# Performance work log

Hardware: AMD Instinct MI355X
Metric: run time of the kernel (lower is better)

Reference implementation:

```python
import jax, jax.numpy as jnp
import numpy as np

NUM_EMBEDDINGS = 8192
EMBEDDING_DIM = 512
COMMITMENT_COST = 0.25
DECAY = 0.99
EPSILON = 1e-05


def _l2_normalize(x, axis=-1, eps=1e-12):
    # matches torch.nn.functional.normalize (p=2)
    n = jnp.sqrt(jnp.sum(x * x, axis=axis, keepdims=True))
    return x / jnp.maximum(n, eps)


def setup_inputs() -> dict:
    key = jax.random.key(0)
    k1, k2, k3 = jax.random.split(key, 3)
    inputs = jax.random.normal(k1, (8, 4096, EMBEDDING_DIM), dtype=jnp.float32)
    embedding = jax.random.normal(k2, (NUM_EMBEDDINGS, EMBEDDING_DIM), dtype=jnp.float32) * 0.01
    ema_cluster_size = jnp.ones((NUM_EMBEDDINGS,), dtype=jnp.float32)
    ema_w = jax.random.normal(k3, (NUM_EMBEDDINGS, EMBEDDING_DIM), dtype=jnp.float32) * 0.01
    return {"inputs": inputs, "embedding": embedding,
            "ema_cluster_size": ema_cluster_size, "ema_w": ema_w}


def reference(inputs, embedding, ema_cluster_size, ema_w):
    K, D = NUM_EMBEDDINGS, EMBEDDING_DIM
    flat = _l2_normalize(inputs.reshape(-1, D))           # [N, D]
    emb_n = _l2_normalize(embedding)                       # [K, D] (in-place normalize in torch)

    # cosine distance: 1 - flat @ emb^T  -> argmin
    distances = 1.0 - jnp.matmul(flat, emb_n.T)            # [N, K]
    idx = jnp.argmin(distances, axis=1)                    # [N]

    # one-hot @ codebook == gather
    quantized = jnp.take(emb_n, idx, axis=0).reshape(inputs.shape)

    # EMA codebook update (training branch), scatter-encode via segment_sum
    counts = jax.ops.segment_sum(jnp.ones_like(idx, dtype=flat.dtype), idx,
                                 num_segments=K)           # [K]
    new_cs = ema_cluster_size * DECAY + (1.0 - DECAY) * counts
    n = jnp.sum(new_cs)
    new_cs = (new_cs + EPSILON) / (n + K * EPSILON) * n
    dw = jax.ops.segment_sum(flat, idx, num_segments=K)    # [K, D] == one_hot^T @ flat
    new_ema_w = ema_w * DECAY + (1.0 - DECAY) * dw
    new_embedding = new_ema_w / jnp.clip(new_cs, EPSILON, None)[:, None]

    e_latent_loss = jnp.mean((jax.lax.stop_gradient(quantized) - inputs) ** 2)
    loss = COMMITMENT_COST * e_latent_loss

    quantized_st = inputs + jax.lax.stop_gradient(quantized - inputs)
    encoding_indices = idx.reshape(inputs.shape[:-1])
    return (quantized_st, loss, encoding_indices, new_cs, new_ema_w, new_embedding)
```

## Files before the change

kernel.cpp:

```cpp
#include <hip/hip_runtime.h>
#include <math.h>

#define NROWS 32768
#define DIM   512
#define KCODE 8192
#define DECAYF 0.99f
#define OMDF   0.01f
#define EPSF   1e-5f
#define COMMITF 0.25f
#define MARGIN 8e-4f

typedef _Float16 half8 __attribute__((ext_vector_type(8)));
typedef _Float16 half4v __attribute__((ext_vector_type(4)));
typedef _Float16 half2v __attribute__((ext_vector_type(2)));
typedef float floatx16 __attribute__((ext_vector_type(16)));


__device__ __forceinline__ float block_sum_256(float v) {
    __shared__ float sm[4];
    int lane = threadIdx.x & 63, wave = threadIdx.x >> 6;
    #pragma unroll
    for (int off = 32; off; off >>= 1) v += __shfl_down(v, off);
    if (lane == 0) sm[wave] = v;
    __syncthreads();
    if (threadIdx.x == 0) v = sm[0] + sm[1] + sm[2] + sm[3];
    return v;
}

__global__ void k_norm_split(const float* __restrict__ src, float* __restrict__ inv,
                             _Float16* __restrict__ hi, _Float16* __restrict__ lo) {
    const int wave = threadIdx.x >> 6;
    const int lane = threadIdx.x & 63;
    const int row = blockIdx.x * 4 + wave;
    const float* p = src + (size_t)row * DIM;
    const float4 f1 = *(const float4*)&p[lane * 4];
    const float4 f2 = *(const float4*)&p[256 + lane * 4];
    float s = f1.x*f1.x + f1.y*f1.y + f1.z*f1.z + f1.w*f1.w
            + f2.x*f2.x + f2.y*f2.y + f2.z*f2.z + f2.w*f2.w;
    #pragma unroll
    for (int off = 32; off; off >>= 1) s += __shfl_down(s, off);
    const float iv = __shfl(1.0f / fmaxf(sqrtf(s), 1e-12f), 0);
    if (lane == 0) inv[row] = iv;

    {
        const float n0 = f1.x * iv, n1 = f1.y * iv, n2 = f1.z * iv, n3 = f1.w * iv;
        const _Float16 h0 = (_Float16)n0, h1 = (_Float16)n1, h2 = (_Float16)n2, h3 = (_Float16)n3;
        half4v hv = {h0, h1, h2, h3};
        *(half4v*)&hi[(size_t)row * DIM + lane * 4] = hv;
        half4v lv = {(_Float16)((n0 - (float)h0) * 4096.f),
                     (_Float16)((n1 - (float)h1) * 4096.f),
                     (_Float16)((n2 - (float)h2) * 4096.f),
                     (_Float16)((n3 - (float)h3) * 4096.f)};
        *(half4v*)&lo[(size_t)row * DIM + lane * 4] = lv;
    }
    {
        const float n0 = f2.x * iv, n1 = f2.y * iv, n2 = f2.z * iv, n3 = f2.w * iv;
        const _Float16 h0 = (_Float16)n0, h1 = (_Float16)n1, h2 = (_Float16)n2, h3 = (_Float16)n3;
        half4v hv = {h0, h1, h2, h3};
        *(half4v*)&hi[(size_t)row * DIM + 256 + lane * 4] = hv;
        half4v lv = {(_Float16)((n0 - (float)h0) * 4096.f),
                     (_Float16)((n1 - (float)h1) * 4096.f),
                     (_Float16)((n2 - (float)h2) * 4096.f),
                     (_Float16)((n3 - (float)h3) * 4096.f)};
        *(half4v*)&lo[(size_t)row * DIM + 256 + lane * 4] = lv;
    }
}

__device__ __forceinline__ void gld16(const _Float16* g, _Float16* l) {
    __builtin_amdgcn_global_load_lds(
        (const __attribute__((address_space(1))) void*)g,
        (__attribute__((address_space(3))) void*)l, 16, 0, 0);
}

__device__ __forceinline__ void top2_upd(float v, int i, float& v1, int& i1, float& v2) {
    if (v > v1) { v2 = v1; v1 = v; i1 = i; }
    else        { v2 = fmaxf(v2, v); }
}

__device__ __forceinline__ void stage_step(const _Float16* __restrict__ Xh,
                                           const _Float16* __restrict__ Eh,
                                           _Float16* dst, int split, int rowBase,
                                           int S, int r0, int ldsOff, int colOff) {
    const int ntB = split * 4096 + (S >> 4) * 256;
    const int col = ((S & 15) << 5) + colOff;
    gld16(Eh + (size_t)(ntB + r0)           * DIM + col, dst + ldsOff);
    gld16(Eh + (size_t)(ntB + 128 + r0)     * DIM + col, dst + 4096 + ldsOff);
    gld16(Xh + (size_t)(rowBase + r0)       * DIM + col, dst + 8192 + ldsOff);
    gld16(Xh + (size_t)(rowBase + 128 + r0) * DIM + col, dst + 12288 + ldsOff);
}

__launch_bounds__(512, 2)
__global__ void k_hi(const _Float16* __restrict__ Xh, const _Float16* __restrict__ Eh,
                     float* __restrict__ sV1, float* __restrict__ sV2,
                     unsigned short* __restrict__ sI1) {
    __shared__ __align__(16) _Float16 lds[4 * 16384];
    __shared__ float mV[256][2], mV2[256][2];
    __shared__ int   mI[256][2];

    const int tid  = threadIdx.x;
    const int w    = tid >> 6;
    const int lane = tid & 63;
    const int wc  = w & 1;
    const int wrr = w >> 1;
    const int c = lane & 31, h = lane >> 5;
    const int rowBase = blockIdx.x * 256;
    const int split   = blockIdx.y;

    const int r0   = tid >> 2;
    const int slot = tid & 3;
    const int Ps   = ((tid >> 2) ^ (tid >> 4)) & 3;
    const int colOff = (slot ^ Ps) * 8;
    const int ldsOff = r0 * 32 + slot * 8;

    const int Pc = (c ^ (c >> 2)) & 3;

    float v1a = -1e30f, v2a = -1e30f, v1b = -1e30f, v2b = -1e30f;
    int i1a = 0, i1b = 0;

    stage_step(Xh, Eh, &lds[0],     split, rowBase, 0, r0, ldsOff, colOff);
    stage_step(Xh, Eh, &lds[16384], split, rowBase, 1, r0, ldsOff, colOff);
    stage_step(Xh, Eh, &lds[32768], split, rowBase, 2, r0, ldsOff, colOff);

    for (int nt = 0; nt < 16; ++nt) {
        const int ntBase = split * 4096 + nt * 256;
        floatx16 acc[4][2];
        #pragma unroll
        for (int i = 0; i < 4; ++i)
            #pragma unroll
            for (int j = 0; j < 2; ++j)
                #pragma unroll
                for (int r = 0; r < 16; ++r) acc[i][j][r] = 0.f;

        #pragma unroll
        for (int k = 0; k < 16; ++k) {
            const int S = nt * 16 + k;
            asm volatile("s_waitcnt vmcnt(8) lgkmcnt(0)" ::: "memory");
            __builtin_amdgcn_s_barrier();
            asm volatile("" ::: "memory");
            stage_step(Xh, Eh, &lds[((k + 3) & 3) * 16384], split, rowBase,
                       (S + 3) & 255, r0, ldsOff, colOff);
            const _Float16* B = &lds[(k & 3) * 16384];
            #pragma unroll
            for (int ks = 0; ks < 2; ++ks) {
                const int so = (((ks << 1) + h) ^ Pc) << 3;
                half8 a0 = *(const half8*)&B[(wc * 128 +  0 + c) * 32 + so];
                half8 a1 = *(const half8*)&B[(wc * 128 + 32 + c) * 32 + so];
                half8 a2 = *(const half8*)&B[(wc * 128 + 64 + c) * 32 + so];
                half8 a3 = *(const half8*)&B[(wc * 128 + 96 + c) * 32 + so];
                half8 b0 = *(const half8*)&B[8192 + (wrr * 64 +  0 + c) * 32 + so];
                half8 b1 = *(const half8*)&B[8192 + (wrr * 64 + 32 + c) * 32 + so];
                __builtin_amdgcn_s_setprio(1);
                acc[0][0] = __builtin_amdgcn_mfma_f32_32x32x16_f16(a0, b0, acc[0][0], 0, 0, 0);
                acc[1][0] = __builtin_amdgcn_mfma_f32_32x32x16_f16(a1, b0, acc[1][0], 0, 0, 0);
                acc[2][0] = __builtin_amdgcn_mfma_f32_32x32x16_f16(a2, b0, acc[2][0], 0, 0, 0);
                acc[3][0] = __builtin_amdgcn_mfma_f32_32x32x16_f16(a3, b0, acc[3][0], 0, 0, 0);
                acc[0][1] = __builtin_amdgcn_mfma_f32_32x32x16_f16(a0, b1, acc[0][1], 0, 0, 0);
                acc[1][1] = __builtin_amdgcn_mfma_f32_32x32x16_f16(a1, b1, acc[1][1], 0, 0, 0);
                acc[2][1] = __builtin_amdgcn_mfma_f32_32x32x16_f16(a2, b1, acc[2][1], 0, 0, 0);
                acc[3][1] = __builtin_amdgcn_mfma_f32_32x32x16_f16(a3, b1, acc[3][1], 0, 0, 0);
                __builtin_amdgcn_s_setprio(0);
            }
        }
        #pragma unroll
        for (int r = 0; r < 16; ++r) {
            const int codeSub = (r & 3) + ((r >> 2) << 3) + (h << 2);
            #pragma unroll
            for (int i = 0; i < 4; ++i) {
                const int code = ntBase + wc * 128 + i * 32 + codeSub;
                top2_upd(acc[i][0][r], code, v1a, i1a, v2a);
                top2_upd(acc[i][1][r], code, v1b, i1b, v2b);
            }
        }
    }

    {
        float ov1 = __shfl_xor(v1a, 32); int oi1 = __shfl_xor(i1a, 32); float ov2 = __shfl_xor(v2a, 32);
        if (ov1 > v1a) { v2a = fmaxf(v1a, ov2); v1a = ov1; i1a = oi1; }
        else if (ov1 == v1a) { v2a = v1a; if (oi1 < i1a) i1a = oi1; }
        else { v2a = fmaxf(v2a, ov1); }
        ov1 = __shfl_xor(v1b, 32); oi1 = __shfl_xor(i1b, 32); ov2 = __shfl_xor(v2b, 32);
        if (ov1 > v1b) { v2b = fmaxf(v1b, ov2); v1b = ov1; i1b = oi1; }
        else if (ov1 == v1b) { v2b = v1b; if (oi1 < i1b) i1b = oi1; }
        else { v2b = fmaxf(v2b, ov1); }
    }
    if (h == 0) {
        const int rA = wrr * 64 + c;
        mV[rA][wc] = v1a; mV2[rA][wc] = v2a; mI[rA][wc] = i1a;
        mV[rA + 32][wc] = v1b; mV2[rA + 32][wc] = v2b; mI[rA + 32][wc] = i1b;
    }
    __syncthreads();
    if (tid < 256) {
        float v1 = mV[tid][0], v2 = mV2[tid][0]; int i1 = mI[tid][0];
        float ov1 = mV[tid][1], ov2 = mV2[tid][1]; int oi1 = mI[tid][1];
        if (ov1 > v1) { v2 = fmaxf(v1, ov2); v1 = ov1; i1 = oi1; }
        else if (ov1 == v1) { v2 = v1; if (oi1 < i1) i1 = oi1; }
        else { v2 = fmaxf(v2, ov1); }
        const int n = rowBase + tid;
        sV1[split * NROWS + n] = v1;
        sV2[split * NROWS + n] = v2;
        sI1[split * NROWS + n] = (unsigned short)i1;
    }
}

__global__ void k_top2_merge(const float* __restrict__ sV1, const float* __restrict__ sV2,
                             const unsigned short* __restrict__ sI1,
                             float* __restrict__ outIdx, int* __restrict__ list,
                             int* __restrict__ flagCnt) {
    const int n = blockIdx.x * 256 + threadIdx.x;
    float a1 = sV1[n], a2 = sV2[n]; int ai = sI1[n];
    float b1 = sV1[NROWS + n], b2 = sV2[NROWS + n]; int bi = sI1[NROWS + n];
    float best, run; int bidx;
    if (b1 > a1) { best = b1; bidx = bi; run = fmaxf(a1, b2); }
    else         { best = a1; bidx = ai; run = fmaxf(a2, b1); }
    outIdx[n] = (float)bidx;
    if (best - run < MARGIN) {
        int p = atomicAdd(flagCnt, 1);
        list[p] = n;
    }
}

__device__ __forceinline__ unsigned long long encodeKey(float v, int idx) {
    unsigned u = __float_as_uint(v);
    u = (u & 0x80000000u) ? ~u : (u | 0x80000000u);
    return ((unsigned long long)u << 32) | (unsigned)(0xFFFFFFFFu - (unsigned)idx);
}

__launch_bounds__(256, 2)
__global__ void k_rescore(const _Float16* __restrict__ Xh, const _Float16* __restrict__ Xl,
                          const _Float16* __restrict__ Eh, const _Float16* __restrict__ El,
                          const int* __restrict__ list, const int* __restrict__ flagCnt,
                          unsigned long long* __restrict__ rkey) {
    const int cnt = *flagCnt;
    const int t = blockIdx.x & 255;
    const int s = blockIdx.x >> 8;
    if (t * 128 >= cnt) return;

    __shared__ __align__(16) _Float16 lds[32768];
    __shared__ float mV[128][2];
    __shared__ int   mI[128][2];

    const int tid  = threadIdx.x;
    const int w    = tid >> 6;
    const int lane = tid & 63;
    const int wc = w & 1, wr = w >> 1;
    const int c = lane & 31, h = lane >> 5;
    const int sr = lane >> 3;
    const int sg = (lane & 7) ^ (sr & 7);
    const int rowA = wc * 64 + c;
    const int rowB = wr * 64 + c;
    const int cx = c & 7;

    int rows_j[4];
    #pragma unroll
    for (int j = 0; j < 4; ++j) {
        const int slot = t * 128 + w * 32 + j * 8 + sr;
        rows_j[j] = (slot < cnt) ? list[slot] : 0;
    }

    float best0 = -1e30f, best1 = -1e30f;
    int bi0 = 0, bi1 = 0;
    const float SC = 1.0f / 4096.0f;

    for (int nt = 0; nt < 4; ++nt) {
        const int ntBase = s * 512 + nt * 128;

        floatx16 accH00, accH01, accH10, accH11, accC00, accC01, accC10, accC11;
        #pragma unroll
        for (int r = 0; r < 16; ++r) {
            accH00[r] = 0.f; accH01[r] = 0.f; accH10[r] = 0.f; accH11[r] = 0.f;
            accC00[r] = 0.f; accC01[r] = 0.f; accC10[r] = 0.f; accC11[r] = 0.f;
        }

        for (int chunk = 0; chunk < 8; ++chunk) {
            const int kt = chunk * 64;
            #pragma unroll
            for (int j = 0; j < 4; ++j) {
                const int rl = w * 32 + j * 8 + sr;
                const size_t gE = (size_t)(ntBase + rl) * DIM + kt + sg * 8;
                const size_t gX = (size_t)rows_j[j] * DIM + kt + sg * 8;
                _Float16* dBase = &lds[(w * 32 + j * 8) * 64];
                gld16(Eh + gE, dBase);
                gld16(El + gE, dBase + 8192);
                gld16(Xh + gX, dBase + 16384);
                gld16(Xl + gX, dBase + 24576);
            }
            __syncthreads();
            #pragma unroll
            for (int ks = 0; ks < 4; ++ks) {
                const int so = ((ks * 2 + h) ^ cx) * 8;
                const half8 ah0 = *(const half8*)&lds[rowA * 64 + so];
                const half8 ah1 = *(const half8*)&lds[(rowA + 32) * 64 + so];
                const half8 al0 = *(const half8*)&lds[8192 + rowA * 64 + so];
                const half8 al1 = *(const half8*)&lds[8192 + (rowA + 32) * 64 + so];
                const half8 bh0 = *(const half8*)&lds[16384 + rowB * 64 + so];
                const half8 bh1 = *(const half8*)&lds[16384 + (rowB + 32) * 64 + so];
                const half8 bl0 = *(const half8*)&lds[24576 + rowB * 64 + so];
                const half8 bl1 = *(const half8*)&lds[24576 + (rowB + 32) * 64 + so];

                accH00 = __builtin_amdgcn_mfma_f32_32x32x16_f16(ah0, bh0, accH00, 0, 0, 0);
                accC00 = __builtin_amdgcn_mfma_f32_32x32x16_f16(ah0, bl0, accC00, 0, 0, 0);
                accC00 = __builtin_amdgcn_mfma_f32_32x32x16_f16(al0, bh0, accC00, 0, 0, 0);

                accH01 = __builtin_amdgcn_mfma_f32_32x32x16_f16(ah0, bh1, accH01, 0, 0, 0);
                accC01 = __builtin_amdgcn_mfma_f32_32x32x16_f16(ah0, bl1, accC01, 0, 0, 0);
                accC01 = __builtin_amdgcn_mfma_f32_32x32x16_f16(al0, bh1, accC01, 0, 0, 0);

                accH10 = __builtin_amdgcn_mfma_f32_32x32x16_f16(ah1, bh0, accH10, 0, 0, 0);
                accC10 = __builtin_amdgcn_mfma_f32_32x32x16_f16(ah1, bl0, accC10, 0, 0, 0);
                accC10 = __builtin_amdgcn_mfma_f32_32x32x16_f16(al1, bh0, accC10, 0, 0, 0);

                accH11 = __builtin_amdgcn_mfma_f32_32x32x16_f16(ah1, bh1, accH11, 0, 0, 0);
                accC11 = __builtin_amdgcn_mfma_f32_32x32x16_f16(ah1, bl1, accC11, 0, 0, 0);
                accC11 = __builtin_amdgcn_mfma_f32_32x32x16_f16(al1, bh1, accC11, 0, 0, 0);
            }
            __syncthreads();
        }

        #pragma unroll
        for (int r = 0; r < 16; ++r) {
            const int codeSub = (r & 3) + ((r >> 2) << 3) + (h << 2);
            const int code0 = ntBase + wc * 64 + codeSub;
            const int code1 = code0 + 32;
            float v;
            v = fmaf(accC00[r], SC, accH00[r]);
            if (v > best0 || (v == best0 && code0 < bi0)) { best0 = v; bi0 = code0; }
            v = fmaf(accC10[r], SC, accH10[r]);
            if (v > best0 || (v == best0 && code1 < bi0)) { best0 = v; bi0 = code1; }
            v = fmaf(accC01[r], SC, accH01[r]);
            if (v > best1 || (v == best1 && code0 < bi1)) { best1 = v; bi1 = code0; }
            v = fmaf(accC11[r], SC, accH11[r]);
            if (v > best1 || (v == best1 && code1 < bi1)) { best1 = v; bi1 = code1; }
        }
    }

    {
        float ov = __shfl_xor(best0, 32); int oi = __shfl_xor(bi0, 32);
        if (ov > best0 || (ov == best0 && oi < bi0)) { best0 = ov; bi0 = oi; }
        ov = __shfl_xor(best1, 32); oi = __shfl_xor(bi1, 32);
        if (ov > best1 || (ov == best1 && oi < bi1)) { best1 = ov; bi1 = oi; }
    }
    if (h == 0) {
        mV[rowB][wc] = best0;      mI[rowB][wc] = bi0;
        mV[rowB + 32][wc] = best1; mI[rowB + 32][wc] = bi1;
    }
    __syncthreads();
    if (tid < 128) {
        const int slot = t * 128 + tid;
        if (slot < cnt) {
            float v0 = mV[tid][0]; int i0 = mI[tid][0];
            float v1 = mV[tid][1]; int i1 = mI[tid][1];
            float bv; int bidx;
            if (v1 > v0 || (v1 == v0 && i1 < i0)) { bv = v1; bidx = i1; }
            else                                  { bv = v0; bidx = i0; }
            atomicMax(&rkey[list[slot]], encodeKey(bv, bidx));
        }
    }
}

__global__ void k_rescore_merge(const unsigned long long* __restrict__ rkey,
                                const int* __restrict__ list, const int* __restrict__ flagCnt,
                                float* __restrict__ outIdx) {
    const int slot = blockIdx.x * 256 + threadIdx.x;
    if (slot < *flagCnt) {
        const int row = list[slot];
        const unsigned long long key = rkey[row];
        const int code = (int)(0xFFFFFFFFu - (unsigned)(key & 0xFFFFFFFFull));
        outIdx[row] = (float)code;
    }
}

__global__ void k_hist(const float* __restrict__ outIdx, int* __restrict__ cntI) {
    const int n = blockIdx.x * 256 + threadIdx.x;
    atomicAdd(&cntI[(int)outIdx[n]], 1);
}

__global__ void k_gather_loss(const float* __restrict__ X, const _Float16* __restrict__ Eh,
                              const _Float16* __restrict__ El, const float* __restrict__ outIdx,
                              float* __restrict__ qst, float* __restrict__ lossAcc) {
    const float SC = 1.0f / 4096.0f;
    float acc = 0.f;
    #pragma unroll
    for (int it = 0; it < 8; ++it) {
        const int e = (it * 2048 + blockIdx.x) * 256 + threadIdx.x;
        const int row = e >> 7;
        const int col = (e & 127) * 4;
        const int k = (int)outIdx[row];
        const float4 x = ((const float4*)X)[e];
        const half4v eh = *(const half4v*)&Eh[(size_t)k * DIM + col];
        const half4v el = *(const half4v*)&El[(size_t)k * DIM + col];
        const float q0 = (float)eh.x + (float)el.x * SC;
        const float q1 = (float)eh.y + (float)el.y * SC;
        const float q2 = (float)eh.z + (float)el.z * SC;
        const float q3 = (float)eh.w + (float)el.w * SC;
        const float d0 = q0 - x.x, d1 = q1 - x.y, d2 = q2 - x.z, d3 = q3 - x.w;
        float4 o; o.x = x.x + d0; o.y = x.y + d1; o.z = x.z + d2; o.w = x.w + d3;
        ((float4*)qst)[e] = o;
        acc += d0 * d0 + d1 * d1 + d2 * d2 + d3 * d3;
    }
    const float ls = block_sum_256(acc);
    if (threadIdx.x == 0) atomicAdd(lossAcc, ls);
}

__global__ void k_cs_pre(const float* __restrict__ emacs, const int* __restrict__ cntI,
                         float* __restrict__ pre, float* __restrict__ nsum) {
    const int k = blockIdx.x * 256 + threadIdx.x;
    float p = emacs[k] * DECAYF + OMDF * (float)cntI[k];
    pre[k] = p;
    float s = block_sum_256(p);
    if (threadIdx.x == 0) atomicAdd(nsum, s);
}

__global__ void k_cs_final(const float* __restrict__ pre, const float* __restrict__ nsum,
                           float* __restrict__ outCS, float* __restrict__ csfin,
                           const float* __restrict__ lossAcc, float* __restrict__ outLoss) {
    const int k = blockIdx.x * 256 + threadIdx.x;
    float n = *nsum;
    float c = (pre[k] + EPSF) / (n + (float)KCODE * EPSF) * n;
    outCS[k] = c;
    csfin[k] = c;
    if (k == 0) *outLoss = COMMITF * (*lossAcc) / (float)(NROWS * DIM);
}

__global__ void k_scan(const int* __restrict__ cntI, int* __restrict__ offs) {
    __shared__ int ps[1024];
    const int t = threadIdx.x;
    int loc[8], pref[8], s = 0;
    #pragma unroll
    for (int j = 0; j < 8; ++j) { loc[j] = cntI[t * 8 + j]; pref[j] = s; s += loc[j]; }
    ps[t] = s;
    __syncthreads();
    for (int d = 1; d < 1024; d <<= 1) {
        int x = (t >= d) ? ps[t - d] : 0;
        __syncthreads();
        ps[t] += x;
        __syncthreads();
    }
    const int base = ps[t] - s;
    #pragma unroll
    for (int j = 0; j < 8; ++j) offs[t * 8 + j] = base + pref[j];
}

__global__ void k_bin(const float* __restrict__ outIdx, const int* __restrict__ offs,
                      int* __restrict__ cursor, int* __restrict__ perm) {
    const int n = blockIdx.x * 256 + threadIdx.x;
    const int k = (int)outIdx[n];
    const int pos = offs[k] + atomicAdd(&cursor[k], 1);
    perm[pos] = n;
}

__global__ void k_dw_fused(const float* __restrict__ X, const float* __restrict__ inv_in,
                           const int* __restrict__ perm, const int* __restrict__ offs,
                           const int* __restrict__ cntI, const float* __restrict__ emaw,
                           const float* __restrict__ csfin,
                           float* __restrict__ outW, float* __restrict__ outE) {
    const int k = blockIdx.x;
    const int t = threadIdx.x;
    const int c = cntI[k];
    const int base = offs[k];
    float a0 = 0.f, a1 = 0.f;
    for (int i = 0; i < c; ++i) {
        const int row = perm[base + i];
        const float iv = inv_in[row];
        const float2 x = *(const float2*)&X[(size_t)row * DIM + t * 2];
        a0 = fmaf(x.x, iv, a0);
        a1 = fmaf(x.y, iv, a1);
    }
    const float2 w2 = *(const float2*)&emaw[(size_t)k * DIM + t * 2];
    const float w0 = w2.x * DECAYF + OMDF * a0;
    const float w1 = w2.y * DECAYF + OMDF * a1;
    float2 ow; ow.x = w0; ow.y = w1;
    *(float2*)&outW[(size_t)k * DIM + t * 2] = ow;
    const float cs = fmaxf(csfin[k], EPSF);
    float2 oe; oe.x = w0 / cs; oe.y = w1 / cs;
    *(float2*)&outE[(size_t)k * DIM + t * 2] = oe;
}

extern "C" void kernel_launch(void* const* d_in, const int* in_sizes, int n_in,
                              void* d_out, int out_size, void* d_ws, size_t ws_size,
                              hipStream_t stream) {
    const float* inputs    = (const float*)d_in[0];
    const float* embedding = (const float*)d_in[1];
    const float* emacs     = (const float*)d_in[2];
    const float* emaw      = (const float*)d_in[3];
    float* out = (float*)d_out;
    float* ws  = (float*)d_ws;

    float* inv_in  = ws;
    float* sV1     = ws + 32768;
    float* sV2     = ws + 98304;
    unsigned short* sI1 = (unsigned short*)(ws + 163840);
    int*   list    = (int*)(ws + 196608);
    int*   flagCnt = (int*)(ws + 229376);
    float* inv_emb = ws + 229440;
    _Float16* Xh   = (_Float16*)(ws + 229440);
    _Float16* Xl   = (_Float16*)(ws + 8618048);
    _Float16* Eh   = (_Float16*)(ws + 17006656);
    _Float16* El   = (_Float16*)(ws + 19103808);
    unsigned long long* rkey = (unsigned long long*)(ws + 32768);
    int*   cntI    = (int*)(ws + 98304);
    int*   cursor  = (int*)(ws + 106496);
    float* lossAcc = ws + 114688;
    float* nsum    = ws + 114689;
    float* pre     = ws + 114692;
    float* csfin   = ws + 122884;
    int*   offs    = (int*)(ws + 131076);
    int*   perm    = (int*)(ws + 139268);

    float* outQst  = out;
    float* outLoss = out + 16777216;
    float* outIdx  = out + 16777217;
    float* outCS   = out + 16809985;
    float* outW    = out + 16818177;
    float* outE    = out + 21012481;

    hipMemsetAsync(flagCnt, 0, sizeof(int), stream);
    k_norm_split<<<KCODE / 4, 256, 0, stream>>>(embedding, inv_emb, Eh, El);
    k_norm_split<<<NROWS / 4, 256, 0, stream>>>(inputs, inv_in, Xh, Xl);
    k_hi<<<dim3(NROWS / 256, 2), 512, 0, stream>>>(Xh, Eh, sV1, sV2, sI1);
    k_top2_merge<<<NROWS / 256, 256, 0, stream>>>(sV1, sV2, sI1, outIdx, list, flagCnt);
    hipMemsetAsync(ws + 32768, 0, (size_t)81922 * sizeof(float), stream);
    k_rescore<<<4096, 256, 0, stream>>>(Xh, Xl, Eh, El, list, flagCnt, rkey);
    k_rescore_merge<<<NROWS / 256, 256, 0, stream>>>(rkey, list, flagCnt, outIdx);
    k_hist<<<NROWS / 256, 256, 0, stream>>>(outIdx, cntI);
    k_gather_loss<<<2048, 256, 0, stream>>>(inputs, Eh, El, outIdx, outQst, lossAcc);
    k_cs_pre<<<KCODE / 256, 256, 0, stream>>>(emacs, cntI, pre, nsum);
    k_cs_final<<<KCODE / 256, 256, 0, stream>>>(pre, nsum, outCS, csfin, lossAcc, outLoss);
    k_scan<<<1, 1024, 0, stream>>>(cntI, offs);
    k_bin<<<NROWS / 256, 256, 0, stream>>>(outIdx, offs, cursor, perm);
    k_dw_fused<<<KCODE, 256, 0, stream>>>(inputs, inv_in, perm, offs, cntI, emaw, csfin,
                                          outW, outE);
}
```

Baseline: 661.5 us.

## Software-pipeline LDS fragment reads ahead of the barrier in the matmul loop

```diff
diff --git a/kernel.cpp b/kernel.cpp
--- a/kernel.cpp
+++ b/kernel.cpp
@@ -89,6 +89,31 @@
     gld16(Xh + (size_t)(rowBase + 128 + r0) * DIM + col, dst + 12288 + ldsOff);
 }
 
+struct FragSet { half8 a0, a1, a2, a3, b0, b1; };
+
+__device__ __forceinline__ void read_frags(const _Float16* __restrict__ B, int ks,
+                                           int wc, int c, int h, int Pc, int wrr,
+                                           FragSet& f) {
+    const int so = (((ks << 1) + h) ^ Pc) << 3;
+    f.a0 = *(const half8*)&B[(wc * 128 +  0 + c) * 32 + so];
+    f.a1 = *(const half8*)&B[(wc * 128 + 32 + c) * 32 + so];
+    f.a2 = *(const half8*)&B[(wc * 128 + 64 + c) * 32 + so];
+    f.a3 = *(const half8*)&B[(wc * 128 + 96 + c) * 32 + so];
+    f.b0 = *(const half8*)&B[8192 + (wrr * 64 +  0 + c) * 32 + so];
+    f.b1 = *(const half8*)&B[8192 + (wrr * 64 + 32 + c) * 32 + so];
+}
+
+__device__ __forceinline__ void mfma8(const FragSet& f, floatx16 acc[4][2]) {
+    acc[0][0] = __builtin_amdgcn_mfma_f32_32x32x16_f16(f.a0, f.b0, acc[0][0], 0, 0, 0);
+    acc[1][0] = __builtin_amdgcn_mfma_f32_32x32x16_f16(f.a1, f.b0, acc[1][0], 0, 0, 0);
+    acc[2][0] = __builtin_amdgcn_mfma_f32_32x32x16_f16(f.a2, f.b0, acc[2][0], 0, 0, 0);
+    acc[3][0] = __builtin_amdgcn_mfma_f32_32x32x16_f16(f.a3, f.b0, acc[3][0], 0, 0, 0);
+    acc[0][1] = __builtin_amdgcn_mfma_f32_32x32x16_f16(f.a0, f.b1, acc[0][1], 0, 0, 0);
+    acc[1][1] = __builtin_amdgcn_mfma_f32_32x32x16_f16(f.a1, f.b1, acc[1][1], 0, 0, 0);
+    acc[2][1] = __builtin_amdgcn_mfma_f32_32x32x16_f16(f.a2, f.b1, acc[2][1], 0, 0, 0);
+    acc[3][1] = __builtin_amdgcn_mfma_f32_32x32x16_f16(f.a3, f.b1, acc[3][1], 0, 0, 0);
+}
+
 __launch_bounds__(512, 2)
 __global__ void k_hi(const _Float16* __restrict__ Xh, const _Float16* __restrict__ Eh,
                      float* __restrict__ sV1, float* __restrict__ sV2,
@@ -120,6 +145,11 @@
     stage_step(Xh, Eh, &lds[0],     split, rowBase, 0, r0, ldsOff, colOff);
     stage_step(Xh, Eh, &lds[16384], split, rowBase, 1, r0, ldsOff, colOff);
     stage_step(Xh, Eh, &lds[32768], split, rowBase, 2, r0, ldsOff, colOff);
+    asm volatile("s_waitcnt vmcnt(4)" ::: "memory");
+    __builtin_amdgcn_s_barrier();
+
+    FragSet fcur, fmid, fnext;
+    read_frags(&lds[0], 0, wc, c, h, Pc, wrr, fcur);
 
     for (int nt = 0; nt < 16; ++nt) {
         const int ntBase = split * 4096 + nt * 256;
@@ -134,32 +164,17 @@
         #pragma unroll
         for (int k = 0; k < 16; ++k) {
             const int S = nt * 16 + k;
-            asm volatile("s_waitcnt vmcnt(8) lgkmcnt(0)" ::: "memory");
-            __builtin_amdgcn_s_barrier();
-            asm volatile("" ::: "memory");
+            read_frags(&lds[((k + 1) & 3) * 16384], 0, wc, c, h, Pc, wrr, fnext);
             stage_step(Xh, Eh, &lds[((k + 3) & 3) * 16384], split, rowBase,
                        (S + 3) & 255, r0, ldsOff, colOff);
-            const _Float16* B = &lds[(k & 3) * 16384];
-            #pragma unroll
-            for (int ks = 0; ks < 2; ++ks) {
-                const int so = (((ks << 1) + h) ^ Pc) << 3;
-                half8 a0 = *(const half8*)&B[(wc * 128 +  0 + c) * 32 + so];
-                half8 a1 = *(const half8*)&B[(wc * 128 + 32 + c) * 32 + so];
-                half8 a2 = *(const half8*)&B[(wc * 128 + 64 + c) * 32 + so];
-                half8 a3 = *(const half8*)&B[(wc * 128 + 96 + c) * 32 + so];
-                half8 b0 = *(const half8*)&B[8192 + (wrr * 64 +  0 + c) * 32 + so];
-                half8 b1 = *(const half8*)&B[8192 + (wrr * 64 + 32 + c) * 32 + so];
-                __builtin_amdgcn_s_setprio(1);
-                acc[0][0] = __builtin_amdgcn_mfma_f32_32x32x16_f16(a0, b0, acc[0][0], 0, 0, 0);
-                acc[1][0] = __builtin_amdgcn_mfma_f32_32x32x16_f16(a1, b0, acc[1][0], 0, 0, 0);
-                acc[2][0] = __builtin_amdgcn_mfma_f32_32x32x16_f16(a2, b0, acc[2][0], 0, 0, 0);
-                acc[3][0] = __builtin_amdgcn_mfma_f32_32x32x16_f16(a3, b0, acc[3][0], 0, 0, 0);
-                acc[0][1] = __builtin_amdgcn_mfma_f32_32x32x16_f16(a0, b1, acc[0][1], 0, 0, 0);
-                acc[1][1] = __builtin_amdgcn_mfma_f32_32x32x16_f16(a1, b1, acc[1][1], 0, 0, 0);
-                acc[2][1] = __builtin_amdgcn_mfma_f32_32x32x16_f16(a2, b1, acc[2][1], 0, 0, 0);
-                acc[3][1] = __builtin_amdgcn_mfma_f32_32x32x16_f16(a3, b1, acc[3][1], 0, 0, 0);
-                __builtin_amdgcn_s_setprio(0);
-            }
+            read_frags(&lds[(k & 3) * 16384], 1, wc, c, h, Pc, wrr, fmid);
+            __builtin_amdgcn_s_setprio(1);
+            mfma8(fcur, acc);
+            mfma8(fmid, acc);
+            __builtin_amdgcn_s_setprio(0);
+            fcur = fnext;
+            asm volatile("s_waitcnt vmcnt(4)" ::: "memory");
+            __builtin_amdgcn_s_barrier();
         }
         #pragma unroll
         for (int r = 0; r < 16; ++r) {
```

Result: slower. 777.9 us (+17.6%).
